# Performance work log

Measured on AMD Instinct MI355X. Metric: run time of the kernel, lower is better.

Reference implementation:

```python
import jax, jax.numpy as jnp
import numpy as np

B, N, E, IN, H, D = 4, 50000, 800000, 128, 4, 32
GAT_SLOPE = 0.2   # DGL GATConv leaky_relu negative_slope
ACT_SLOPE = 0.01  # nn.LeakyReLU default
BN_EPS = 1e-5


def _leaky(x, slope):
    return jnp.where(x >= 0, x, slope * x)


def setup_inputs() -> dict:
    key = jax.random.key(0)
    ks = jax.random.split(key, 6)
    xx = jax.random.normal(ks[0], (B, N, IN), dtype=jnp.float32)
    W = jax.random.normal(ks[1], (IN, H * D), dtype=jnp.float32) / np.sqrt(IN).astype(np.float32)
    attn_l = jax.random.normal(ks[2], (H, D), dtype=jnp.float32) * 0.1
    attn_r = jax.random.normal(ks[3], (H, D), dtype=jnp.float32) * 0.1
    gamma = jnp.ones((H * D,), dtype=jnp.float32)
    beta = jnp.zeros((H * D,), dtype=jnp.float32)
    src = jax.random.randint(ks[4], (E,), 0, N, dtype=jnp.int32)
    dst = jax.random.randint(ks[5], (E,), 0, N, dtype=jnp.int32)
    return {"xx": xx, "W": W, "attn_l": attn_l, "attn_r": attn_r,
            "gamma": gamma, "beta": beta, "src": src, "dst": dst}


def reference(xx, W, attn_l, attn_r, gamma, beta, src, dst):
    def gat_single(x):  # x: [N, IN]
        feat = (x @ W).reshape(N, H, D)                       # [N,H,D]
        el = jnp.einsum('nhd,hd->nh', feat, attn_l)           # [N,H]
        er = jnp.einsum('nhd,hd->nh', feat, attn_r)           # [N,H]
        e = _leaky(el[src] + er[dst], GAT_SLOPE)              # [E,H]
        # edge softmax over incoming edges of each dst node (stable)
        m = jax.ops.segment_max(e, dst, num_segments=N)       # [N,H]
        m = jnp.where(jnp.isfinite(m), m, 0.0)                # zero-in-degree guard
        w = jnp.exp(e - m[dst])                               # [E,H]
        denom = jax.ops.segment_sum(w, dst, num_segments=N)   # [N,H]
        alpha = w / jnp.maximum(denom[dst], 1e-9)             # [E,H]
        # scatter-weighted aggregation
        msg = alpha[:, :, None] * feat[src]                   # [E,H,D]
        return jax.ops.segment_sum(msg, dst, num_segments=N)  # [N,H,D]

    out = jax.vmap(gat_single)(xx)                            # [B,N,H,D]
    h = out.reshape(B, N, H * D)                              # flatten(2)
    # BatchNorm1d over channel dim (stats over B and N), training-mode batch stats
    mean = h.mean(axis=(0, 1))
    var = h.var(axis=(0, 1))
    hn = (h - mean) * jax.lax.rsqrt(var + BN_EPS) * gamma + beta
    return _leaky(hn, ACT_SLOPE)                              # [B,N,H*D]
```

## Files before the change

kernel.cpp:

```cpp
#include <hip/hip_runtime.h>
#include <math.h>

#define B_ 4
#define N_ 50000
#define E_ 800000
#define IN_ 128
#define H_ 4
#define D_ 32
#define HD_ 128
#define M_ (B_*N_)
#define GR_ 32
#define GEMM_BLOCKS 512

constexpr float GAT_SLOPE = 0.2f;
constexpr float ACT_SLOPE = 0.01f;
constexpr float BN_EPS = 1e-5f;

__device__ __forceinline__ unsigned short f2bf(float x) {
    unsigned u = __float_as_uint(x);
    unsigned r = (u + 0x7FFFu + ((u >> 16) & 1u)) >> 16;
    return (unsigned short)r;
}
__device__ __forceinline__ float bflo(unsigned u) {
    return __uint_as_float(u << 16);
}
__device__ __forceinline__ float bfhi(unsigned u) {
    return __uint_as_float(u & 0xFFFF0000u);
}

__global__ __launch_bounds__(256) void gemm_kernel(const float* __restrict__ xx,
                                                   const float* __restrict__ W,
                                                   const float* __restrict__ al,
                                                   const float* __restrict__ ar,
                                                   unsigned short* __restrict__ featb,
                                                   float* __restrict__ el,
                                                   float* __restrict__ er) {
    __shared__ float Ws[IN_ * HD_];
    __shared__ float Xs[GR_][IN_];
    const int tid = threadIdx.x;
    const int cl = tid & 31;
    const int r0 = (tid >> 5) * 4;

    for (int i = tid; i < IN_ * HD_ / 4; i += 256)
        ((float4*)Ws)[i] = ((const float4*)W)[i];

    const float4 alv = *(const float4*)&al[4 * cl];
    const float4 arv = *(const float4*)&ar[4 * cl];

    for (int tt = blockIdx.x; tt < M_ / GR_; tt += GEMM_BLOCKS) {
        const long row0 = (long)tt * GR_;
        __syncthreads();
        for (int i = tid; i < GR_ * IN_ / 4; i += 256)
            ((float4*)Xs)[i] = ((const float4*)(xx + row0 * IN_))[i];
        __syncthreads();

        float acc[4][4] = {};
#pragma unroll 4
        for (int k = 0; k < IN_; k += 4) {
            float4 w0 = *(const float4*)&Ws[(k + 0) * HD_ + 4 * cl];
            float4 w1 = *(const float4*)&Ws[(k + 1) * HD_ + 4 * cl];
            float4 w2 = *(const float4*)&Ws[(k + 2) * HD_ + 4 * cl];
            float4 w3 = *(const float4*)&Ws[(k + 3) * HD_ + 4 * cl];
#pragma unroll
            for (int i = 0; i < 4; ++i) {
                float4 xv = *(const float4*)&Xs[r0 + i][k];
                acc[i][0] = fmaf(xv.x, w0.x, acc[i][0]);
                acc[i][1] = fmaf(xv.x, w0.y, acc[i][1]);
                acc[i][2] = fmaf(xv.x, w0.z, acc[i][2]);
                acc[i][3] = fmaf(xv.x, w0.w, acc[i][3]);
                acc[i][0] = fmaf(xv.y, w1.x, acc[i][0]);
                acc[i][1] = fmaf(xv.y, w1.y, acc[i][1]);
                acc[i][2] = fmaf(xv.y, w1.z, acc[i][2]);
                acc[i][3] = fmaf(xv.y, w1.w, acc[i][3]);
                acc[i][0] = fmaf(xv.z, w2.x, acc[i][0]);
                acc[i][1] = fmaf(xv.z, w2.y, acc[i][1]);
                acc[i][2] = fmaf(xv.z, w2.z, acc[i][2]);
                acc[i][3] = fmaf(xv.z, w2.w, acc[i][3]);
                acc[i][0] = fmaf(xv.w, w3.x, acc[i][0]);
                acc[i][1] = fmaf(xv.w, w3.y, acc[i][1]);
                acc[i][2] = fmaf(xv.w, w3.z, acc[i][2]);
                acc[i][3] = fmaf(xv.w, w3.w, acc[i][3]);
            }
        }

#pragma unroll
        for (int i = 0; i < 4; ++i) {
            long r = row0 + r0 + i;
            ushort4 pv;
            pv.x = f2bf(acc[i][0]); pv.y = f2bf(acc[i][1]);
            pv.z = f2bf(acc[i][2]); pv.w = f2bf(acc[i][3]);
            *(ushort4*)&featb[r * HD_ + 4 * cl] = pv;
            float pl = acc[i][0] * alv.x + acc[i][1] * alv.y + acc[i][2] * alv.z + acc[i][3] * alv.w;
            float pr = acc[i][0] * arv.x + acc[i][1] * arv.y + acc[i][2] * arv.z + acc[i][3] * arv.w;
#pragma unroll
            for (int o = 4; o; o >>= 1) {
                pl += __shfl_xor(pl, o, 64);
                pr += __shfl_xor(pr, o, 64);
            }
            if ((cl & 7) == 0) {
                int h = cl >> 3;
                el[r * H_ + h] = pl;
                er[r * H_ + h] = pr;
            }
        }
    }
}

__global__ __launch_bounds__(256) void hist_kernel(const int* __restrict__ dst,
                                                   int* __restrict__ counts) {
    for (int e = blockIdx.x * 256 + threadIdx.x; e < E_; e += gridDim.x * 256)
        atomicAdd(&counts[dst[e]], 1);
}

__global__ __launch_bounds__(1024) void scan_kernel(const int* __restrict__ counts,
                                                    int* __restrict__ offsets,
                                                    int* __restrict__ cursor) {
    __shared__ int part[1024];
    const int tid = threadIdx.x;
    const int CH = (N_ + 1023) / 1024;
    const int base = tid * CH;
    int s = 0;
    for (int i = 0; i < CH; ++i) {
        int idx = base + i;
        if (idx < N_) s += counts[idx];
    }
    part[tid] = s;
    __syncthreads();
    for (int off = 1; off < 1024; off <<= 1) {
        int v = (tid >= off) ? part[tid - off] : 0;
        __syncthreads();
        part[tid] += v;
        __syncthreads();
    }
    int run = (tid == 0) ? 0 : part[tid - 1];
    for (int i = 0; i < CH; ++i) {
        int idx = base + i;
        if (idx < N_) {
            offsets[idx] = run;
            cursor[idx] = run;
            run += counts[idx];
        }
    }
    if (tid == 0) offsets[N_] = part[1023];
}

__global__ __launch_bounds__(256) void scatter_kernel(const int* __restrict__ src,
                                                      const int* __restrict__ dst,
                                                      int* __restrict__ cursor,
                                                      int* __restrict__ srcs) {
    for (int e = blockIdx.x * 256 + threadIdx.x; e < E_; e += gridDim.x * 256) {
        int pos = atomicAdd(&cursor[dst[e]], 1);
        srcs[pos] = src[e];
    }
}

__global__ __launch_bounds__(64) void aggregate_kernel(const int* __restrict__ offsets,
                                                       const int* __restrict__ srcs,
                                                       const float* __restrict__ el,
                                                       const float* __restrict__ er,
                                                       const unsigned short* __restrict__ featb,
                                                       float* __restrict__ out) {
    const int t = threadIdx.x;
    const int h = t >> 4;
    const int hb = t & 48;
    const int t4 = 4 * t;
    const unsigned g = blockIdx.x;
    const int xcd = (int)(g & 7u);
    const int b = xcd >> 1;
    const int n = (int)((g >> 3) * 2 + (xcd & 1));
    const long bbase = (long)b * N_;
    const int beg = offsets[n], end = offsets[n + 1];

    const float ern = er[(bbase + n) * H_ + h];
    const char* fbase = (const char*)(featb + bbase * HD_);
    const int j16 = t & 15;

    float acc0 = 0.f, acc1 = 0.f, dsum = 0.f;
    for (int c0 = beg; c0 < end; c0 += 16) {
        const int cnt = min(16, end - c0);
        float w = 0.f;
        int off = 0;
        if (j16 < cnt) {
            int s = srcs[c0 + j16];
            off = s << 8;
            float ev = el[(bbase + s) * H_ + h] + ern;
            ev = ev >= 0.f ? ev : GAT_SLOPE * ev;
            w = __expf(ev);
        }
        dsum += w;
        int j = 0;
        for (; j + 3 < cnt; j += 4) {
            int o0 = __shfl(off, j);
            int o1 = __shfl(off, j + 1);
            int o2 = __shfl(off, j + 2);
            int o3 = __shfl(off, j + 3);
            float w0 = __shfl(w, hb | j);
            float w1 = __shfl(w, hb | (j + 1));
            float w2 = __shfl(w, hb | (j + 2));
            float w3 = __shfl(w, hb | (j + 3));
            unsigned u0 = *(const unsigned*)(fbase + o0 + t4);
            unsigned u1 = *(const unsigned*)(fbase + o1 + t4);
            unsigned u2 = *(const unsigned*)(fbase + o2 + t4);
            unsigned u3 = *(const unsigned*)(fbase + o3 + t4);
            acc0 = fmaf(w0, bflo(u0), acc0); acc1 = fmaf(w0, bfhi(u0), acc1);
            acc0 = fmaf(w1, bflo(u1), acc0); acc1 = fmaf(w1, bfhi(u1), acc1);
            acc0 = fmaf(w2, bflo(u2), acc0); acc1 = fmaf(w2, bfhi(u2), acc1);
            acc0 = fmaf(w3, bflo(u3), acc0); acc1 = fmaf(w3, bfhi(u3), acc1);
        }
        for (; j < cnt; ++j) {
            int o0 = __shfl(off, j);
            float w0 = __shfl(w, hb | j);
            unsigned u0 = *(const unsigned*)(fbase + o0 + t4);
            acc0 = fmaf(w0, bflo(u0), acc0);
            acc1 = fmaf(w0, bfhi(u0), acc1);
        }
    }
#pragma unroll
    for (int o = 8; o; o >>= 1) dsum += __shfl_xor(dsum, o, 64);
    const float inv = 1.0f / fmaxf(dsum, 1e-9f);
    float2 res = make_float2(acc0 * inv, acc1 * inv);
    *(float2*)&out[((bbase + n) * HD_) + 2 * t] = res;
}

__global__ __launch_bounds__(256) void stats_kernel(const float* __restrict__ out,
                                                    float* __restrict__ chsum) {
    const int tid = threadIdx.x;
    const int c = tid & 127;
    const int half = tid >> 7;
    float s = 0.f, s2 = 0.f;
    for (long rp = blockIdx.x; rp < M_ / 2; rp += gridDim.x) {
        long row = rp * 2 + half;
        float v = out[row * HD_ + c];
        s += v;
        s2 += v * v;
    }
    __shared__ float red[512];
    red[tid] = s; red[256 + tid] = s2;
    __syncthreads();
    if (tid < 128) {
        s = red[tid] + red[tid + 128];
        s2 = red[256 + tid] + red[256 + tid + 128];
        atomicAdd(&chsum[c], s);
        atomicAdd(&chsum[128 + c], s2);
    }
}

__global__ void params_kernel(const float* __restrict__ chsum,
                              const float* __restrict__ gamma,
                              const float* __restrict__ beta,
                              float* __restrict__ ss) {
    int c = threadIdx.x;
    float mean = chsum[c] / (float)M_;
    float var = chsum[128 + c] / (float)M_ - mean * mean;
    float rstd = rsqrtf(var + BN_EPS);
    float sc = rstd * gamma[c];
    ss[c] = sc;
    ss[128 + c] = beta[c] - mean * sc;
}

__global__ __launch_bounds__(256) void norm_kernel(float* __restrict__ out,
                                                   const float* __restrict__ ss) {
    __shared__ float s_sc[128], s_sh[128];
    if (threadIdx.x < 128) {
        s_sc[threadIdx.x] = ss[threadIdx.x];
        s_sh[threadIdx.x] = ss[128 + threadIdx.x];
    }
    __syncthreads();
    const long total4 = (long)M_ * HD_ / 4;
    for (long i = (long)blockIdx.x * 256 + threadIdx.x; i < total4;
         i += (long)gridDim.x * 256) {
        float4 v = ((float4*)out)[i];
        int c = (int)((i & 31) << 2);
        float4 r;
        r.x = v.x * s_sc[c + 0] + s_sh[c + 0];
        r.y = v.y * s_sc[c + 1] + s_sh[c + 1];
        r.z = v.z * s_sc[c + 2] + s_sh[c + 2];
        r.w = v.w * s_sc[c + 3] + s_sh[c + 3];
        r.x = r.x >= 0.f ? r.x : ACT_SLOPE * r.x;
        r.y = r.y >= 0.f ? r.y : ACT_SLOPE * r.y;
        r.z = r.z >= 0.f ? r.z : ACT_SLOPE * r.z;
        r.w = r.w >= 0.f ? r.w : ACT_SLOPE * r.w;
        ((float4*)out)[i] = r;
    }
}

extern "C" void kernel_launch(void* const* d_in, const int* in_sizes, int n_in,
                              void* d_out, int out_size, void* d_ws, size_t ws_size,
                              hipStream_t stream) {
    const float* xx    = (const float*)d_in[0];
    const float* W     = (const float*)d_in[1];
    const float* al    = (const float*)d_in[2];
    const float* ar    = (const float*)d_in[3];
    const float* gamma = (const float*)d_in[4];
    const float* beta  = (const float*)d_in[5];
    const int*   src   = (const int*)d_in[6];
    const int*   dst   = (const int*)d_in[7];
    float* out = (float*)d_out;

    char* ws = (char*)d_ws;
    unsigned short* featb = (unsigned short*)ws; ws += (size_t)M_ * HD_ * 2;
    float* el      = (float*)ws;  ws += (size_t)M_ * H_ * 4;
    float* er      = (float*)ws;  ws += (size_t)M_ * H_ * 4;
    int*   counts  = (int*)ws;    ws += (size_t)N_ * 4;
    int*   offsets = (int*)ws;    ws += (size_t)(N_ + 1) * 4;
    int*   cursor  = (int*)ws;    ws += (size_t)N_ * 4;
    int*   srcs    = (int*)ws;    ws += (size_t)E_ * 4;
    float* chsum   = (float*)ws;  ws += 256 * 4;
    float* ss      = (float*)ws;  ws += 256 * 4;

    hipMemsetAsync(counts, 0, (size_t)N_ * 4, stream);
    hipMemsetAsync(chsum, 0, 256 * 4, stream);

    gemm_kernel<<<GEMM_BLOCKS, 256, 0, stream>>>(xx, W, al, ar, featb, el, er);
    hist_kernel<<<2048, 256, 0, stream>>>(dst, counts);
    scan_kernel<<<1, 1024, 0, stream>>>(counts, offsets, cursor);
    scatter_kernel<<<2048, 256, 0, stream>>>(src, dst, cursor, srcs);
    aggregate_kernel<<<M_, 64, 0, stream>>>(offsets, srcs, el, er, featb, out);
    stats_kernel<<<2048, 256, 0, stream>>>(out, chsum);
    params_kernel<<<1, 128, 0, stream>>>(chsum, gamma, beta, ss);
    norm_kernel<<<4096, 256, 0, stream>>>(out, ss);
}
```

Measured before the change: 704.8 us.

## Use bf16 MFMA for projection GEMM and split attention logits into separate kernel

Replaces the fp32 FMA projection GEMM with a bf16 MFMA 16x16x32 kernel that stages W (transposed) and a 64-row x tile in swizzled LDS, one block per 64 rows. The el/er attention dot products move out of the GEMM epilogue into a new kernel that re-reads the bf16 features. The goal is to cut GEMM compute time on the matrix cores. In exchange, inputs are rounded to bf16 before the multiply, el/er are now computed from bf16-rounded features, each block reconverts W, and there is an extra launch plus an extra read of the feature buffer.

```diff
diff --git a/kernel.cpp b/kernel.cpp
--- a/kernel.cpp
+++ b/kernel.cpp
@@ -9,99 +9,102 @@
 #define D_ 32
 #define HD_ 128
 #define M_ (B_*N_)
-#define GR_ 32
-#define GEMM_BLOCKS 512
+#define GT_ (M_/64)
 
 constexpr float GAT_SLOPE = 0.2f;
 constexpr float ACT_SLOPE = 0.01f;
 constexpr float BN_EPS = 1e-5f;
 
+typedef __attribute__((ext_vector_type(8))) short bf16x8;
+typedef __attribute__((ext_vector_type(4))) float f32x4;
+
+#define SWZ(r, b) ((b) ^ (((r) & 7) << 4))
+
 __device__ __forceinline__ unsigned short f2bf(float x) {
     unsigned u = __float_as_uint(x);
-    unsigned r = (u + 0x7FFFu + ((u >> 16) & 1u)) >> 16;
-    return (unsigned short)r;
-}
-__device__ __forceinline__ float bflo(unsigned u) {
-    return __uint_as_float(u << 16);
-}
-__device__ __forceinline__ float bfhi(unsigned u) {
-    return __uint_as_float(u & 0xFFFF0000u);
-}
+    return (unsigned short)((u + 0x7FFFu + ((u >> 16) & 1u)) >> 16);
+}
+__device__ __forceinline__ float bf2f(unsigned short h) {
+    return __uint_as_float(((unsigned)h) << 16);
+}
+__device__ __forceinline__ float bflo(unsigned u) { return __uint_as_float(u << 16); }
+__device__ __forceinline__ float bfhi(unsigned u) { return __uint_as_float(u & 0xFFFF0000u); }
 
 __global__ __launch_bounds__(256) void gemm_kernel(const float* __restrict__ xx,
                                                    const float* __restrict__ W,
-                                                   const float* __restrict__ al,
-                                                   const float* __restrict__ ar,
-                                                   unsigned short* __restrict__ featb,
-                                                   float* __restrict__ el,
-                                                   float* __restrict__ er) {
-    __shared__ float Ws[IN_ * HD_];
-    __shared__ float Xs[GR_][IN_];
+                                                   unsigned short* __restrict__ featb) {
+    __shared__ __align__(16) char WtL[128 * 256];
+    __shared__ __align__(16) char XsL[64 * 256];
     const int tid = threadIdx.x;
-    const int cl = tid & 31;
-    const int r0 = (tid >> 5) * 4;
-
-    for (int i = tid; i < IN_ * HD_ / 4; i += 256)
-        ((float4*)Ws)[i] = ((const float4*)W)[i];
-
-    const float4 alv = *(const float4*)&al[4 * cl];
-    const float4 arv = *(const float4*)&ar[4 * cl];
-
-    for (int tt = blockIdx.x; tt < M_ / GR_; tt += GEMM_BLOCKS) {
-        const long row0 = (long)tt * GR_;
-        __syncthreads();
-        for (int i = tid; i < GR_ * IN_ / 4; i += 256)
-            ((float4*)Xs)[i] = ((const float4*)(xx + row0 * IN_))[i];
-        __syncthreads();
-
-        float acc[4][4] = {};
-#pragma unroll 4
-        for (int k = 0; k < IN_; k += 4) {
-            float4 w0 = *(const float4*)&Ws[(k + 0) * HD_ + 4 * cl];
-            float4 w1 = *(const float4*)&Ws[(k + 1) * HD_ + 4 * cl];
-            float4 w2 = *(const float4*)&Ws[(k + 2) * HD_ + 4 * cl];
-            float4 w3 = *(const float4*)&Ws[(k + 3) * HD_ + 4 * cl];
-#pragma unroll
-            for (int i = 0; i < 4; ++i) {
-                float4 xv = *(const float4*)&Xs[r0 + i][k];
-                acc[i][0] = fmaf(xv.x, w0.x, acc[i][0]);
-                acc[i][1] = fmaf(xv.x, w0.y, acc[i][1]);
-                acc[i][2] = fmaf(xv.x, w0.z, acc[i][2]);
-                acc[i][3] = fmaf(xv.x, w0.w, acc[i][3]);
-                acc[i][0] = fmaf(xv.y, w1.x, acc[i][0]);
-                acc[i][1] = fmaf(xv.y, w1.y, acc[i][1]);
-                acc[i][2] = fmaf(xv.y, w1.z, acc[i][2]);
-                acc[i][3] = fmaf(xv.y, w1.w, acc[i][3]);
-                acc[i][0] = fmaf(xv.z, w2.x, acc[i][0]);
-                acc[i][1] = fmaf(xv.z, w2.y, acc[i][1]);
-                acc[i][2] = fmaf(xv.z, w2.z, acc[i][2]);
-                acc[i][3] = fmaf(xv.z, w2.w, acc[i][3]);
-                acc[i][0] = fmaf(xv.w, w3.x, acc[i][0]);
-                acc[i][1] = fmaf(xv.w, w3.y, acc[i][1]);
-                acc[i][2] = fmaf(xv.w, w3.z, acc[i][2]);
-                acc[i][3] = fmaf(xv.w, w3.w, acc[i][3]);
-            }
-        }
-
-#pragma unroll
-        for (int i = 0; i < 4; ++i) {
-            long r = row0 + r0 + i;
-            ushort4 pv;
-            pv.x = f2bf(acc[i][0]); pv.y = f2bf(acc[i][1]);
-            pv.z = f2bf(acc[i][2]); pv.w = f2bf(acc[i][3]);
-            *(ushort4*)&featb[r * HD_ + 4 * cl] = pv;
-            float pl = acc[i][0] * alv.x + acc[i][1] * alv.y + acc[i][2] * alv.z + acc[i][3] * alv.w;
-            float pr = acc[i][0] * arv.x + acc[i][1] * arv.y + acc[i][2] * arv.z + acc[i][3] * arv.w;
-#pragma unroll
-            for (int o = 4; o; o >>= 1) {
-                pl += __shfl_xor(pl, o, 64);
-                pr += __shfl_xor(pr, o, 64);
-            }
-            if ((cl & 7) == 0) {
-                int h = cl >> 3;
-                el[r * H_ + h] = pl;
-                er[r * H_ + h] = pr;
-            }
+    const int lane = tid & 63;
+    const int wv = tid >> 6;
+    const int lr = lane & 15;
+    const int lq = lane >> 4;
+    const int arow = wv * 16 + lr;
+    const long row0 = (long)blockIdx.x * 64;
+
+    for (int i = tid; i < IN_ * HD_ / 4; i += 256) {
+        int k = i >> 5;
+        int c0 = (i & 31) << 2;
+        float4 v = ((const float4*)W)[i];
+        unsigned short p[4] = {f2bf(v.x), f2bf(v.y), f2bf(v.z), f2bf(v.w)};
+#pragma unroll
+        for (int j = 0; j < 4; ++j) {
+            int c = c0 + j;
+            *(unsigned short*)(WtL + SWZ(c, c * 256 + k * 2)) = p[j];
+        }
+    }
+    for (int i = tid; i < 64 * IN_ / 4; i += 256) {
+        int r = i >> 5;
+        int c0 = (i & 31) << 2;
+        float4 v = ((const float4*)(xx + row0 * IN_))[i];
+        ushort4 p;
+        p.x = f2bf(v.x); p.y = f2bf(v.y); p.z = f2bf(v.z); p.w = f2bf(v.w);
+        *(ushort4*)(XsL + SWZ(r, r * 256 + c0 * 2)) = p;
+    }
+    __syncthreads();
+
+    f32x4 acc[8] = {};
+#pragma unroll
+    for (int ks = 0; ks < 4; ++ks) {
+        bf16x8 a = *(const bf16x8*)(XsL + SWZ(arow, arow * 256 + ks * 64 + lq * 16));
+#pragma unroll
+        for (int nt = 0; nt < 8; ++nt) {
+            int br = nt * 16 + lr;
+            bf16x8 b = *(const bf16x8*)(WtL + SWZ(br, br * 256 + ks * 64 + lq * 16));
+            acc[nt] = __builtin_amdgcn_mfma_f32_16x16x32_bf16(a, b, acc[nt], 0, 0, 0);
+        }
+    }
+
+    unsigned short* fout = featb + (row0 + wv * 16 + lq * 4) * HD_ + lr;
+#pragma unroll
+    for (int nt = 0; nt < 8; ++nt)
+#pragma unroll
+        for (int r = 0; r < 4; ++r)
+            fout[r * HD_ + nt * 16] = f2bf(acc[nt][r]);
+}
+
+__global__ __launch_bounds__(256) void elr_kernel(const unsigned short* __restrict__ featb,
+                                                  const float* __restrict__ al,
+                                                  const float* __restrict__ ar,
+                                                  float* __restrict__ el,
+                                                  float* __restrict__ er) {
+    const int tid = threadIdx.x;
+    const int c = tid & 127;
+    const int h = c >> 5, d = c & 31;
+    const int half = tid >> 7;
+    for (long rp = blockIdx.x; rp < M_ / 2; rp += gridDim.x) {
+        long row = rp * 2 + half;
+        float f = bf2f(featb[row * HD_ + c]);
+        float pl = f * al[c];
+        float pr = f * ar[c];
+        for (int o = 16; o; o >>= 1) {
+            pl += __shfl_down(pl, o, 32);
+            pr += __shfl_down(pr, o, 32);
+        }
+        if (d == 0) {
+            el[row * H_ + h] = pl;
+            er[row * H_ + h] = pr;
         }
     }
 }
@@ -311,7 +314,8 @@
     hipMemsetAsync(counts, 0, (size_t)N_ * 4, stream);
     hipMemsetAsync(chsum, 0, 256 * 4, stream);
 
-    gemm_kernel<<<GEMM_BLOCKS, 256, 0, stream>>>(xx, W, al, ar, featb, el, er);
+    gemm_kernel<<<GT_, 256, 0, stream>>>(xx, W, featb);
+    elr_kernel<<<4096, 256, 0, stream>>>(featb, al, ar, el, er);
     hist_kernel<<<2048, 256, 0, stream>>>(dst, counts);
     scan_kernel<<<1, 1024, 0, stream>>>(counts, offsets, cursor);
     scatter_kernel<<<2048, 256, 0, stream>>>(src, dst, cursor, srcs);
```

New measurement: 718.4 us. Within noise of the previous version (+1.9%).
